# Performance work log

Hardware: AMD Instinct MI355X
Metric: run time of the kernel (lower is better)

The kernel has to match this reference:

```python
import jax, jax.numpy as jnp
import numpy as np

B, C, H, W, R = 4, 128, 64, 256, 8  # batch, channels, height, width, window radius


def setup_inputs() -> dict:
    key = jax.random.key(0)
    k0, k1, k2, k3 = jax.random.split(key, 4)
    feature = jax.random.normal(k0, (B, C, H, W), dtype=jnp.float32)
    position = 0.02 * jax.random.normal(k1, (B, C, H, W), dtype=jnp.float32)
    # 1x1 conv weights (xavier-like scale), bias zeros as in nn.Conv2d default-ish
    Wq = jax.random.normal(k2, (C, C), dtype=jnp.float32) / np.float32(np.sqrt(C))
    Wk = jax.random.normal(k3, (C, C), dtype=jnp.float32) / np.float32(np.sqrt(C))
    bq = jnp.zeros((C,), dtype=jnp.float32)
    bk = jnp.zeros((C,), dtype=jnp.float32)
    return {"feature": feature, "position": position, "Wq": Wq, "bq": bq, "Wk": Wk, "bk": bk}


def reference(feature, position, Wq, bq, Wk, bk):
    # feature/position: [b, c, h, w]
    f = feature + position
    b, c, h, w = f.shape
    # 1x1 convs == channel matmuls
    q = jnp.einsum('oc,bchw->bohw', Wq, f) + bq[None, :, None, None]
    k = jnp.einsum('oc,bchw->bohw', Wk, f) + bk[None, :, None, None]
    r = R
    Kw = 2 * r + 1
    # pad along width, gather sliding windows: [b, c, h, w, Kw]
    kp = jnp.pad(k, ((0, 0), (0, 0), (0, 0), (r, r)))
    vp = jnp.pad(f, ((0, 0), (0, 0), (0, 0), (r, r)))
    idx = jnp.arange(w)[:, None] + jnp.arange(Kw)[None, :]  # [w, Kw]
    kwin = kp[:, :, :, idx]
    vwin = vp[:, :, :, idx]
    scale = jnp.asarray(np.sqrt(c), dtype=q.dtype)
    scores = jnp.einsum('bchw,bchwk->bhwk', q, kwin) / scale  # [b, h, w, Kw]
    attn = jax.nn.softmax(scores, axis=-1)
    out = jnp.einsum('bhwk,bchwk->bchw', attn, vwin)
    return out
```

## Files before the change

### kernel.cpp

```cpp
#include <hip/hip_runtime.h>
#include <hip/hip_bf16.h>
#include <math.h>

#define BB 4
#define CCH 128
#define HH 64
#define WW 256
#define RR 8
#define KWIN 17
#define TW 32
#define TWH 48
#define NTHREADS 256
#define PIT 136
#define FAP 48
#define PTP 48
#define PT_HI 5440
#define MROWS 144

typedef __attribute__((ext_vector_type(8))) short short8;
typedef __attribute__((ext_vector_type(4))) short short4v;
typedef __attribute__((ext_vector_type(4))) float f32x4;

__device__ __forceinline__ short f2bf(float x) {
    union { __hip_bfloat16 b; short s; } u;
    u.b = __float2bfloat16(x);
    return u.s;
}

__global__ __launch_bounds__(256)
void prep_kernel(const float* __restrict__ Wq, const float* __restrict__ bq,
                 const float* __restrict__ Wk, short* __restrict__ Mp)
{
    const int t = threadIdx.x;
    const int r = blockIdx.x * 2 + (t >> 7);
    const int c = t & 127;
    float a0 = 0.f, a1 = 0.f, a2 = 0.f, a3 = 0.f;
    if (r < CCH) {
        #pragma unroll
        for (int j = 0; j < CCH; j += 4) {
            a0 = fmaf(Wq[(j + 0) * CCH + r], Wk[(j + 0) * CCH + c], a0);
            a1 = fmaf(Wq[(j + 1) * CCH + r], Wk[(j + 1) * CCH + c], a1);
            a2 = fmaf(Wq[(j + 2) * CCH + r], Wk[(j + 2) * CCH + c], a2);
            a3 = fmaf(Wq[(j + 3) * CCH + r], Wk[(j + 3) * CCH + c], a3);
        }
    } else if (r == CCH) {
        #pragma unroll
        for (int o = 0; o < CCH; o += 4) {
            a0 = fmaf(bq[o + 0], Wk[(o + 0) * CCH + c], a0);
            a1 = fmaf(bq[o + 1], Wk[(o + 1) * CCH + c], a1);
            a2 = fmaf(bq[o + 2], Wk[(o + 2) * CCH + c], a2);
            a3 = fmaf(bq[o + 3], Wk[(o + 3) * CCH + c], a3);
        }
    }
    Mp[r * CCH + c] = f2bf((a0 + a1) + (a2 + a3));
}

#define ST_IDX(r) (((r) >> 4) * 1088 + ((r) & 15) * 36)

__global__ __launch_bounds__(NTHREADS, 4)
void attn1d_fused(const float* __restrict__ feature,
                  const float* __restrict__ position,
                  const short* __restrict__ Mp,
                  float* __restrict__ out)
{
    __shared__ __align__(16) char uA[TWH * PIT * 2];
    __shared__ __align__(16) char uB[TWH * PIT * 2];
    __shared__ __align__(16) short fA[CCH][FAP];
    __shared__ float ubias[TWH];
    short (*fBt)[PIT] = (short(*)[PIT])uA;
    short (*gT)[PIT]  = (short(*)[PIT])uB;
    float* Stp        = (float*)uB;
    short* uAs        = (short*)uA;

    const int t    = threadIdx.x;
    const int wid  = t >> 6;
    const int lane = t & 63;
    const int lrow = lane & 15;
    const int lgrp = lane >> 4;

    int blk = blockIdx.x;
    blk = (blk & 7) * 256 + (blk >> 3);
    const int wt = blk & 7;
    const int bh = blk >> 3;
    const int h  = bh & (HH - 1);
    const int b  = bh >> 6;
    const int w0 = wt * TW - RR;
    const int base = ((b * CCH) * HH + h) * WW;

    const int mrow = wid * 32;
    short8 Mf[2][4];
    #pragma unroll
    for (int mf = 0; mf < 2; ++mf)
        #pragma unroll
        for (int kk = 0; kk < 4; ++kk)
            Mf[mf][kk] = *(const short8*)(Mp + (mrow + mf * 16 + lrow) * CCH
                                             + kk * 32 + lgrp * 8);
    short8 Mf2[4];
    if (wid == 3) {
        #pragma unroll
        for (int kk = 0; kk < 4; ++kk)
            Mf2[kk] = *(const short8*)(Mp + (CCH + lrow) * CCH + kk * 32 + lgrp * 8);
    }

    #pragma unroll
    for (int i = 0; i < 6; ++i) {
        const int idx = i * NTHREADS + t;
        const int c  = idx / 12;
        const int wq = idx - c * 12;
        const int w  = w0 + wq * 4;
        float4 fv = {0.f, 0.f, 0.f, 0.f};
        if (w >= 0 && w < WW) {
            const int off = base + c * (HH * WW) + w;
            const float4 fa = *(const float4*)(feature + off);
            const float4 pa = *(const float4*)(position + off);
            fv.x = fa.x + pa.x; fv.y = fa.y + pa.y;
            fv.z = fa.z + pa.z; fv.w = fa.w + pa.w;
        }
        short4v s4;
        s4[0] = f2bf(fv.x); s4[1] = f2bf(fv.y); s4[2] = f2bf(fv.z); s4[3] = f2bf(fv.w);
        *(short4v*)&fA[c][wq * 4] = s4;
        fBt[wq * 4 + 0][c] = s4[0];
        fBt[wq * 4 + 1][c] = s4[1];
        fBt[wq * 4 + 2][c] = s4[2];
        fBt[wq * 4 + 3][c] = s4[3];
    }
    __syncthreads();

    {
        f32x4 acc[2][3];
        #pragma unroll
        for (int mf = 0; mf < 2; ++mf)
            #pragma unroll
            for (int nf = 0; nf < 3; ++nf)
                acc[mf][nf] = (f32x4){0.f, 0.f, 0.f, 0.f};
        f32x4 acc2[3];
        #pragma unroll
        for (int nf = 0; nf < 3; ++nf) acc2[nf] = (f32x4){0.f, 0.f, 0.f, 0.f};

        #pragma unroll
        for (int kk = 0; kk < 4; ++kk) {
            short8 bfr[3];
            #pragma unroll
            for (int nf = 0; nf < 3; ++nf)
                bfr[nf] = *(const short8*)&fBt[nf * 16 + lrow][kk * 32 + lgrp * 8];
            #pragma unroll
            for (int mf = 0; mf < 2; ++mf)
                #pragma unroll
                for (int nf = 0; nf < 3; ++nf)
                    acc[mf][nf] = __builtin_amdgcn_mfma_f32_16x16x32_bf16(
                        Mf[mf][kk], bfr[nf], acc[mf][nf], 0, 0, 0);
            if (wid == 3) {
                #pragma unroll
                for (int nf = 0; nf < 3; ++nf)
                    acc2[nf] = __builtin_amdgcn_mfma_f32_16x16x32_bf16(
                        Mf2[kk], bfr[nf], acc2[nf], 0, 0, 0);
            }
        }

        #pragma unroll
        for (int mf = 0; mf < 2; ++mf)
            #pragma unroll
            for (int nf = 0; nf < 3; ++nf) {
                short4v s;
                #pragma unroll
                for (int reg = 0; reg < 4; ++reg)
                    s[reg] = f2bf(acc[mf][nf][reg]);
                *(short4v*)&gT[nf * 16 + lrow][mrow + mf * 16 + lgrp * 4] = s;
            }
        if (wid == 3 && lgrp == 0) {
            const float isc = 0.08838834764831845f;
            #pragma unroll
            for (int nf = 0; nf < 3; ++nf)
                ubias[nf * 16 + lrow] = acc2[nf][0] * isc;
        }
    }
    __syncthreads();

    if (wid < 3) {
        const int nf = wid;
        f32x4 s0 = {0.f,0.f,0.f,0.f}, s1 = {0.f,0.f,0.f,0.f};
        #pragma unroll
        for (int kk = 0; kk < 4; ++kk) {
            const short8 a0 = *(const short8*)&fBt[RR + lrow     ][kk * 32 + lgrp * 8];
            const short8 a1 = *(const short8*)&fBt[RR + 16 + lrow][kk * 32 + lgrp * 8];
            const short8 bb = *(const short8*)&gT[nf * 16 + lrow][kk * 32 + lgrp * 8];
            s0 = __builtin_amdgcn_mfma_f32_16x16x32_bf16(a0, bb, s0, 0, 0, 0);
            s1 = __builtin_amdgcn_mfma_f32_16x16x32_bf16(a1, bb, s1, 0, 0, 0);
        }
        const float isc = 0.08838834764831845f;
        const int sb = ST_IDX(nf * 16 + lrow);
        *(f32x4*)&Stp[sb + lgrp * 4]      = s0 * isc;
        *(f32x4*)&Stp[sb + 16 + lgrp * 4] = s1 * isc;
    } else {
        const short8 z = {0,0,0,0,0,0,0,0};
        #pragma unroll
        for (int i = 0; i < 2; ++i) {
            const int q8 = i * 64 + lane;
            if (q8 < 96) {
                *(short8*)(uAs + q8 * 8) = z;
                *(short8*)(uAs + PT_HI + q8 * 8) = z;
            }
        }
    }
    __syncthreads();

    if (t < TW * 4) {
        const int w = t >> 2, g = t & 3;
        const int nt = (g == 0) ? 5 : 4;
        const int prow = (w < 16) ? (w * PTP) : (PT_HI + (w - 16) * PTP);
        float sv[5];
        float mx = -3.0e38f;
        #pragma unroll
        for (int i = 0; i < 5; ++i) {
            if (i < nt) {
                const int j = (i == 4) ? 16 : (g + i * 4);
                const int r = w + j;
                sv[i] = Stp[ST_IDX(r) + w] + ubias[r];
                mx = fmaxf(mx, sv[i]);
            }
        }
        mx = fmaxf(mx, __shfl_xor(mx, 1, 4));
        mx = fmaxf(mx, __shfl_xor(mx, 2, 4));
        float sum = 0.f;
        #pragma unroll
        for (int i = 0; i < 5; ++i)
            if (i < nt) { sv[i] = __expf(sv[i] - mx); sum += sv[i]; }
        sum += __shfl_xor(sum, 1, 4);
        sum += __shfl_xor(sum, 2, 4);
        const float inv = 1.f / sum;
        #pragma unroll
        for (int i = 0; i < 5; ++i)
            if (i < nt) {
                const int j = (i == 4) ? 16 : (g + i * 4);
                uAs[prow + w + j] = f2bf(sv[i] * inv);
            }
    }
    __syncthreads();

    {
        const int cb = wid * 32;
        const short8 z = {0,0,0,0,0,0,0,0};
        f32x4 d00 = {0.f,0.f,0.f,0.f}, d01 = d00, d10 = d00, d11 = d00;
        #pragma unroll
        for (int kk = 0; kk < 2; ++kk) {
            const int koff = kk * 32 + lgrp * 8;
            const bool live = (koff < TWH);
            short8 a0 = z, a1 = z, b0 = z, b1 = z;
            if (live) {
                a0 = *(const short8*)&fA[cb + lrow     ][koff];
                a1 = *(const short8*)&fA[cb + 16 + lrow][koff];
                b0 = *(const short8*)(uAs + lrow * PTP + koff);
                b1 = *(const short8*)(uAs + PT_HI + lrow * PTP + koff);
            }
            d00 = __builtin_amdgcn_mfma_f32_16x16x32_bf16(a0, b0, d00, 0, 0, 0);
            d01 = __builtin_amdgcn_mfma_f32_16x16x32_bf16(a0, b1, d01, 0, 0, 0);
            d10 = __builtin_amdgcn_mfma_f32_16x16x32_bf16(a1, b0, d10, 0, 0, 0);
            d11 = __builtin_amdgcn_mfma_f32_16x16x32_bf16(a1, b1, d11, 0, 0, 0);
        }
        const int wbase = wt * TW;
        #pragma unroll
        for (int reg = 0; reg < 4; ++reg) {
            const int c0 = cb + lgrp * 4 + reg;
            out[base + c0 * (HH * WW)        + wbase + lrow]      = d00[reg];
            out[base + c0 * (HH * WW)        + wbase + 16 + lrow] = d01[reg];
            out[base + (c0 + 16) * (HH * WW) + wbase + lrow]      = d10[reg];
            out[base + (c0 + 16) * (HH * WW) + wbase + 16 + lrow] = d11[reg];
        }
    }
}

extern "C" void kernel_launch(void* const* d_in, const int* in_sizes, int n_in,
                              void* d_out, int out_size, void* d_ws, size_t ws_size,
                              hipStream_t stream) {
    const float* feature  = (const float*)d_in[0];
    const float* position = (const float*)d_in[1];
    const float* Wq = (const float*)d_in[2];
    const float* bq = (const float*)d_in[3];
    const float* Wk = (const float*)d_in[4];
    const float* bk = (const float*)d_in[5];
    (void)bk;
    float* out = (float*)d_out;
    short* Mp  = (short*)d_ws;

    prep_kernel<<<MROWS / 2, 256, 0, stream>>>(Wq, bq, Wk, Mp);
    const dim3 grid(BB * HH * (WW / TW));
    attn1d_fused<<<grid, NTHREADS, 0, stream>>>(feature, position, Mp, out);
}
```

Before: 35.86 us.

## Drop channel-major fA LDS copy, gather A fragments from transposed tile, raise occupancy

```diff
diff --git a/kernel.cpp b/kernel.cpp
--- a/kernel.cpp
+++ b/kernel.cpp
@@ -12,9 +12,7 @@
 #define TWH 48
 #define NTHREADS 256
 #define PIT 136
-#define FAP 48
-#define PTP 48
-#define PT_HI 5440
+#define PTP 56
 #define MROWS 144
 
 typedef __attribute__((ext_vector_type(8))) short short8;
@@ -57,20 +55,18 @@
 
 #define ST_IDX(r) (((r) >> 4) * 1088 + ((r) & 15) * 36)
 
-__global__ __launch_bounds__(NTHREADS, 4)
+__global__ __launch_bounds__(NTHREADS, 5)
 void attn1d_fused(const float* __restrict__ feature,
                   const float* __restrict__ position,
                   const short* __restrict__ Mp,
                   float* __restrict__ out)
 {
-    __shared__ __align__(16) char uA[TWH * PIT * 2];
-    __shared__ __align__(16) char uB[TWH * PIT * 2];
-    __shared__ __align__(16) short fA[CCH][FAP];
+    __shared__ __align__(16) short fBt[TWH][PIT];
+    __shared__ __align__(16) char  uB[TWH * PIT * 2];
+    __shared__ __align__(16) short Pt[TW][PTP];
     __shared__ float ubias[TWH];
-    short (*fBt)[PIT] = (short(*)[PIT])uA;
     short (*gT)[PIT]  = (short(*)[PIT])uB;
     float* Stp        = (float*)uB;
-    short* uAs        = (short*)uA;
 
     const int t    = threadIdx.x;
     const int wid  = t >> 6;
@@ -116,13 +112,10 @@
             fv.x = fa.x + pa.x; fv.y = fa.y + pa.y;
             fv.z = fa.z + pa.z; fv.w = fa.w + pa.w;
         }
-        short4v s4;
-        s4[0] = f2bf(fv.x); s4[1] = f2bf(fv.y); s4[2] = f2bf(fv.z); s4[3] = f2bf(fv.w);
-        *(short4v*)&fA[c][wq * 4] = s4;
-        fBt[wq * 4 + 0][c] = s4[0];
-        fBt[wq * 4 + 1][c] = s4[1];
-        fBt[wq * 4 + 2][c] = s4[2];
-        fBt[wq * 4 + 3][c] = s4[3];
+        fBt[wq * 4 + 0][c] = f2bf(fv.x);
+        fBt[wq * 4 + 1][c] = f2bf(fv.y);
+        fBt[wq * 4 + 2][c] = f2bf(fv.z);
+        fBt[wq * 4 + 3][c] = f2bf(fv.w);
     }
     __syncthreads();
 
@@ -193,13 +186,11 @@
         *(f32x4*)&Stp[sb + 16 + lgrp * 4] = s1 * isc;
     } else {
         const short8 z = {0,0,0,0,0,0,0,0};
-        #pragma unroll
-        for (int i = 0; i < 2; ++i) {
+        short* p = &Pt[0][0];
+        #pragma unroll
+        for (int i = 0; i < 4; ++i) {
             const int q8 = i * 64 + lane;
-            if (q8 < 96) {
-                *(short8*)(uAs + q8 * 8) = z;
-                *(short8*)(uAs + PT_HI + q8 * 8) = z;
-            }
+            if (q8 < (TW * PTP) / 8) *(short8*)(p + q8 * 8) = z;
         }
     }
     __syncthreads();
@@ -207,7 +198,6 @@
     if (t < TW * 4) {
         const int w = t >> 2, g = t & 3;
         const int nt = (g == 0) ? 5 : 4;
-        const int prow = (w < 16) ? (w * PTP) : (PT_HI + (w - 16) * PTP);
         float sv[5];
         float mx = -3.0e38f;
         #pragma unroll
@@ -232,7 +222,7 @@
         for (int i = 0; i < 5; ++i)
             if (i < nt) {
                 const int j = (i == 4) ? 16 : (g + i * 4);
-                uAs[prow + w + j] = f2bf(sv[i] * inv);
+                Pt[w][w + j] = f2bf(sv[i] * inv);
             }
     }
     __syncthreads();
@@ -247,10 +237,13 @@
             const bool live = (koff < TWH);
             short8 a0 = z, a1 = z, b0 = z, b1 = z;
             if (live) {
-                a0 = *(const short8*)&fA[cb + lrow     ][koff];
-                a1 = *(const short8*)&fA[cb + 16 + lrow][koff];
-                b0 = *(const short8*)(uAs + lrow * PTP + koff);
-                b1 = *(const short8*)(uAs + PT_HI + lrow * PTP + koff);
+                #pragma unroll
+                for (int j = 0; j < 8; ++j) {
+                    a0[j] = fBt[koff + j][cb + lrow];
+                    a1[j] = fBt[koff + j][cb + 16 + lrow];
+                }
+                b0 = *(const short8*)&Pt[lrow][koff];
+                b1 = *(const short8*)&Pt[16 + lrow][koff];
             }
             d00 = __builtin_amdgcn_mfma_f32_16x16x32_bf16(a0, b0, d00, 0, 0, 0);
             d01 = __builtin_amdgcn_mfma_f32_16x16x32_bf16(a0, b1, d01, 0, 0, 0);
```

Result: slower. 43.36 us (+20.9%).
